# Kernel optimization log

Hardware: AMD Instinct MI355X
Metric: run time of the kernel (lower is better)

The kernel has to match this reference:

```python
import jax, jax.numpy as jnp
import numpy as np

C = 1024
FACTOR = 4
C_INT = C * FACTOR


def setup_inputs() -> dict:
    key = jax.random.key(0)
    ks = jax.random.split(key, 6)
    act = jax.random.normal(ks[0], (4, 2048, C), dtype=jnp.float32)
    mask = jnp.ones((4, 2048), dtype=jnp.float32)
    # LayerNorm params
    ln_scale = jnp.ones((C,), dtype=jnp.float32)
    ln_bias = jnp.zeros((C,), dtype=jnp.float32)
    # Linear 1 (init='linear'): lecun-normal-ish
    w1 = jax.random.normal(ks[1], (C, C_INT), dtype=jnp.float32) / np.sqrt(C)
    b1 = jnp.zeros((C_INT,), dtype=jnp.float32)
    # Linear 2 (init='final' -> zeros in AF2; use small random so grads are nontrivial)
    w2 = jax.random.normal(ks[2], (C_INT, C), dtype=jnp.float32) * 0.02
    b2 = jnp.zeros((C,), dtype=jnp.float32)
    return {"act": act, "mask": mask, "ln_scale": ln_scale, "ln_bias": ln_bias,
            "w1": w1, "b1": b1, "w2": w2, "b2": b2}


def _layernorm(x, scale, bias, eps=1e-5):
    mu = jnp.mean(x, axis=-1, keepdims=True)
    var = jnp.mean(jnp.square(x - mu), axis=-1, keepdims=True)
    return (x - mu) * jax.lax.rsqrt(var + eps) * scale + bias


def reference(act, mask, ln_scale, ln_bias, w1, b1, w2, b2):
    # mask is accepted but unused, matching the original forward.
    x = _layernorm(act, ln_scale, ln_bias)
    h = jax.nn.relu(jnp.einsum('bsc,cf->bsf', x, w1) + b1)
    return jnp.einsum('bsf,fc->bsc', h, w2) + b2
```

## Files before the change

### kernel.cpp

```cpp
#include <hip/hip_runtime.h>
#include <hip/hip_bf16.h>
#include <cstdint>

typedef unsigned short u16;
typedef __bf16 bf16x8 __attribute__((ext_vector_type(8)));
typedef float floatx4 __attribute__((ext_vector_type(4)));

#define AS1 __attribute__((address_space(1)))
#define AS3 __attribute__((address_space(3)))

static __device__ __forceinline__ u16 f2bf(float f) {
    union { float f; unsigned int u; } v; v.f = f;
    unsigned int u = v.u;
    return (u16)((u + 0x7FFFu + ((u >> 16) & 1u)) >> 16);
}

static __device__ __forceinline__ void bar() {
    __builtin_amdgcn_sched_barrier(0);
    asm volatile("" ::: "memory");
    __builtin_amdgcn_s_barrier();
    asm volatile("" ::: "memory");
    __builtin_amdgcn_sched_barrier(0);
}

__device__ __forceinline__ void transpose_body(
    const float* __restrict__ in, u16* __restrict__ out,
    int R, int Ccols, int bx, int by, int tid, float (*tile)[33])
{
    const int tx = tid & 31;
    const int ty = tid >> 5;
    const int c0 = bx * 32;
    const int r0 = by * 32;
#pragma unroll
    for (int i = 0; i < 32; i += 8)
        tile[ty + i][tx] = in[(size_t)(r0 + ty + i) * Ccols + (c0 + tx)];
    __syncthreads();
#pragma unroll
    for (int i = 0; i < 32; i += 8)
        out[(size_t)(c0 + ty + i) * R + (r0 + tx)] = f2bf(tile[tx][ty + i]);
}

__global__ __launch_bounds__(256)
void prep(const float* __restrict__ w1, const float* __restrict__ w2,
          const float* __restrict__ act, const float* __restrict__ ln_scale,
          const float* __restrict__ ln_bias,
          u16* __restrict__ W1t, u16* __restrict__ W2t, u16* __restrict__ X)
{
    __shared__ float smem[32][33];
    const int id  = blockIdx.x;
    const int tid = threadIdx.x;

    if (id < 4096) {
        transpose_body(w1, W1t, 1024, 4096, id & 127, id >> 7, tid, smem);
        return;
    }
    if (id < 8192) {
        const int t = id - 4096;
        transpose_body(w2, W2t, 4096, 1024, t & 31, t >> 5, tid, smem);
        return;
    }
    const int row = id - 8192;
    const float4 v = ((const float4*)(act + (size_t)row * 1024))[tid];
    float s  = v.x + v.y + v.z + v.w;
    float ss = v.x * v.x + v.y * v.y + v.z * v.z + v.w * v.w;
#pragma unroll
    for (int off = 32; off > 0; off >>= 1) {
        s  += __shfl_xor(s, off, 64);
        ss += __shfl_xor(ss, off, 64);
    }
    float* red = &smem[0][0];
    const int wave = tid >> 6, lane = tid & 63;
    if (lane == 0) { red[wave] = s; red[4 + wave] = ss; }
    __syncthreads();
    s  = red[0] + red[1] + red[2] + red[3];
    ss = red[4] + red[5] + red[6] + red[7];
    const float mu  = s * (1.0f / 1024.0f);
    const float var = ss * (1.0f / 1024.0f) - mu * mu;
    const float rs  = rsqrtf(var + 1e-5f);
    const float4 sc = ((const float4*)ln_scale)[tid];
    const float4 bi = ((const float4*)ln_bias)[tid];
    ushort4 o;
    o.x = f2bf((v.x - mu) * rs * sc.x + bi.x);
    o.y = f2bf((v.y - mu) * rs * sc.y + bi.y);
    o.z = f2bf((v.z - mu) * rs * sc.z + bi.z);
    o.w = f2bf((v.w - mu) * rs * sc.w + bi.w);
    ((ushort4*)(X + (size_t)row * 1024))[tid] = o;
}

template <bool BF16_OUT, bool RELU>
__global__ __launch_bounds__(512, 2)
void gemm256(const u16* __restrict__ A,
             const u16* __restrict__ Bt,
             const float* __restrict__ bias,
             void* __restrict__ Cout,
             int M, int N, int K)
{
    constexpr int BM = 256, BN = 128, BK = 64;
    constexpr int ASZ = BM * BK;
    constexpr int BSZ = BN * BK;
    __shared__ __align__(16) u16 Alds[3 * ASZ];
    __shared__ __align__(16) u16 Blds[3 * BSZ];

    const int tid  = threadIdx.x;
    const int wave = tid >> 6;
    const int lane = tid & 63;
    const int srow = lane >> 3;
    const int s_st = lane & 7;
    const int quad = lane >> 4;
    const int l16  = lane & 15;
    const int rkey = l16 & 7;
    const int wm   = wave >> 1;
    const int wn   = wave & 1;

    const int nbm = M >> 8;
    const int id  = blockIdx.x;
    const int bm  = id % nbm;
    const int bn  = id / nbm;

    const u16* Ag = A  + (size_t)bm * BM * K;
    const u16* Bg = Bt + (size_t)bn * BN * K;

    auto stageA = [&](int r, int k0, int ab) {
        const int ca  = wave * 4 + r;
        const int row = ca * 8 + srow;
        const int col = (s_st ^ (row & 7)) * 8;
        __builtin_amdgcn_global_load_lds(
            (AS1 void*)(Ag + (size_t)row * K + k0 + col),
            (AS3 void*)(&Alds[ab + ca * 512]), 16, 0, 0);
    };
    auto stageB = [&](int r, int k0, int bb) {
        const int cb  = wave * 2 + r;
        const int row = cb * 8 + srow;
        const int col = (s_st ^ (row & 7)) * 8;
        __builtin_amdgcn_global_load_lds(
            (AS1 void*)(Bg + (size_t)row * K + k0 + col),
            (AS3 void*)(&Blds[bb + cb * 512]), 16, 0, 0);
    };

    floatx4 acc[4][4];
#pragma unroll
    for (int i = 0; i < 4; ++i)
#pragma unroll
        for (int j = 0; j < 4; ++j)
            acc[i][j] = (floatx4){0.f, 0.f, 0.f, 0.f};

    const int NT = K >> 6;

#pragma unroll
    for (int r = 0; r < 4; ++r) stageA(r, 0, 0);
#pragma unroll
    for (int r = 0; r < 2; ++r) stageB(r, 0, 0);
#pragma unroll
    for (int r = 0; r < 4; ++r) stageA(r, BK, ASZ);
#pragma unroll
    for (int r = 0; r < 2; ++r) stageB(r, BK, BSZ);
    asm volatile("s_waitcnt vmcnt(6)" ::: "memory");
    bar();

    int bsel = 0;
    for (int t = 0; t < NT; ++t) {
        const int ab  = bsel * ASZ;
        const int bb  = bsel * BSZ;
        const int bs2 = (bsel >= 1) ? bsel - 1 : 2;
        const int ab2 = bs2 * ASZ;
        const int bb2 = bs2 * BSZ;
        const bool do_stage = (t + 2 < NT);
        const int  k2 = (t + 2) << 6;

#pragma unroll
        for (int kk = 0; kk < 2; ++kk) {
            const int slot = ((kk * 4 + quad) ^ rkey) * 8;
            bf16x8 afr[4], bfr[4];
#pragma unroll
            for (int i = 0; i < 4; ++i) {
                afr[i] = *(const bf16x8*)
                    &Alds[ab + (wm * 64 + i * 16 + l16) * 64 + slot];
                bfr[i] = *(const bf16x8*)
                    &Blds[bb + (wn * 64 + i * 16 + l16) * 64 + slot];
            }
            if (do_stage) {
                stageA(kk * 2 + 0, k2, ab2);
                stageA(kk * 2 + 1, k2, ab2);
                stageB(kk, k2, bb2);
            }
            bar();
            __builtin_amdgcn_s_setprio(1);
#pragma unroll
            for (int mi = 0; mi < 4; ++mi)
#pragma unroll
                for (int ni = 0; ni < 4; ++ni)
                    acc[mi][ni] = __builtin_amdgcn_mfma_f32_16x16x32_bf16(
                        bfr[ni], afr[mi], acc[mi][ni], 0, 0, 0);
            __builtin_amdgcn_s_setprio(0);
            if (kk == 1) {
                if (do_stage)
                    asm volatile("s_waitcnt vmcnt(6)" ::: "memory");
                else if (t + 1 < NT)
                    asm volatile("s_waitcnt vmcnt(0)" ::: "memory");
            }
            bar();
        }
        bsel = (bsel == 2) ? 0 : bsel + 1;
    }

    const int mbase = bm * BM + wm * 64;
    const int nbase = bn * BN + wn * 64;
#pragma unroll
    for (int mi = 0; mi < 4; ++mi) {
        const int m = mbase + mi * 16 + l16;
#pragma unroll
        for (int ni = 0; ni < 4; ++ni) {
            const int n0 = nbase + ni * 16 + quad * 4;
            const float4 bv = *(const float4*)&bias[n0];
            float v0 = acc[mi][ni][0] + bv.x;
            float v1 = acc[mi][ni][1] + bv.y;
            float v2 = acc[mi][ni][2] + bv.z;
            float v3 = acc[mi][ni][3] + bv.w;
            if (RELU) {
                v0 = fmaxf(v0, 0.f); v1 = fmaxf(v1, 0.f);
                v2 = fmaxf(v2, 0.f); v3 = fmaxf(v3, 0.f);
            }
            if (BF16_OUT) {
                ushort4 o = { f2bf(v0), f2bf(v1), f2bf(v2), f2bf(v3) };
                *(ushort4*)&((u16*)Cout)[(size_t)m * N + n0] = o;
            } else {
                float4 o = { v0, v1, v2, v3 };
                *(float4*)&((float*)Cout)[(size_t)m * N + n0] = o;
            }
        }
    }
}

extern "C" void kernel_launch(void* const* d_in, const int* in_sizes, int n_in,
                              void* d_out, int out_size, void* d_ws, size_t ws_size,
                              hipStream_t stream)
{
    const float* act      = (const float*)d_in[0];
    const float* ln_scale = (const float*)d_in[2];
    const float* ln_bias  = (const float*)d_in[3];
    const float* w1       = (const float*)d_in[4];
    const float* b1       = (const float*)d_in[5];
    const float* w2       = (const float*)d_in[6];
    const float* b2       = (const float*)d_in[7];
    float* out = (float*)d_out;

    const int M = 8192, C = 1024, CI = 4096;

    u16* X   = (u16*)d_ws;
    u16* W1t = X   + (size_t)M * C;
    u16* W2t = W1t + (size_t)CI * C;
    u16* H   = W2t + (size_t)C * CI;

    prep<<<16384, 256, 0, stream>>>(w1, w2, act, ln_scale, ln_bias, W1t, W2t, X);
    gemm256<true, true><<<(M / 256) * (CI / 128), 512, 0, stream>>>(
        X, W1t, b1, (void*)H, M, CI, C);
    gemm256<false, false><<<(M / 256) * (C / 128), 512, 0, stream>>>(
        H, W2t, b2, (void*)out, M, C, CI);
}
```

Before: 278.4 us.

## Templatize GEMM tile width, switch to double buffering with per-tile barrier

Makes the GEMM kernel's N-tile width a template parameter and uses a 256x256 tile for the first GEMM, so each wave computes an 8x4 fragment grid with more A/B reuse. The triple-buffered pipeline with two barriers per K-step and partial vmcnt waits is replaced by a double buffer: the next tile is prefetched at the start of each iteration, followed by a full vmcnt(0) wait and one barrier at the end. B fragments are held in registers across the M loop. The aim is higher arithmetic intensity and fewer barriers. The cost is more accumulator registers, less overlap of loads with compute, and fewer blocks for the first GEMM.

```diff
diff --git a/kernel.cpp b/kernel.cpp
--- a/kernel.cpp
+++ b/kernel.cpp
@@ -87,19 +87,27 @@
     ((ushort4*)(X + (size_t)row * 1024))[tid] = o;
 }
 
-template <bool BF16_OUT, bool RELU>
+template <int BN, bool BF16_OUT, bool RELU>
 __global__ __launch_bounds__(512, 2)
-void gemm256(const u16* __restrict__ A,
+void gemm_v8(const u16* __restrict__ A,
              const u16* __restrict__ Bt,
              const float* __restrict__ bias,
              void* __restrict__ Cout,
              int M, int N, int K)
 {
-    constexpr int BM = 256, BN = 128, BK = 64;
-    constexpr int ASZ = BM * BK;
-    constexpr int BSZ = BN * BK;
-    __shared__ __align__(16) u16 Alds[3 * ASZ];
-    __shared__ __align__(16) u16 Blds[3 * BSZ];
+    constexpr int BM   = 256, BK = 64;
+    constexpr int WN   = BN / 64;
+    constexpr int WM   = 8 / WN;
+    constexpr int WTM  = BM / WM;
+    constexpr int MF_M = WTM / 16;
+    constexpr int MF_N = 4;
+    constexpr int ASZ  = BM * BK;
+    constexpr int BSZ  = BN * BK;
+    constexpr int NCA  = BM / 64;
+    constexpr int NCB  = BN / 64;
+
+    __shared__ __align__(16) u16 Alds[2 * ASZ];
+    __shared__ __align__(16) u16 Blds[2 * BSZ];
 
     const int tid  = threadIdx.x;
     const int wave = tid >> 6;
@@ -109,8 +117,8 @@
     const int quad = lane >> 4;
     const int l16  = lane & 15;
     const int rkey = l16 & 7;
-    const int wm   = wave >> 1;
-    const int wn   = wave & 1;
+    const int wm   = wave / WN;
+    const int wn   = wave % WN;
 
     const int nbm = M >> 8;
     const int id  = blockIdx.x;
@@ -121,7 +129,7 @@
     const u16* Bg = Bt + (size_t)bn * BN * K;
 
     auto stageA = [&](int r, int k0, int ab) {
-        const int ca  = wave * 4 + r;
+        const int ca  = wave * NCA + r;
         const int row = ca * 8 + srow;
         const int col = (s_st ^ (row & 7)) * 8;
         __builtin_amdgcn_global_load_lds(
@@ -129,7 +137,7 @@
             (AS3 void*)(&Alds[ab + ca * 512]), 16, 0, 0);
     };
     auto stageB = [&](int r, int k0, int bb) {
-        const int cb  = wave * 2 + r;
+        const int cb  = wave * NCB + r;
         const int row = cb * 8 + srow;
         const int col = (s_st ^ (row & 7)) * 8;
         __builtin_amdgcn_global_load_lds(
@@ -137,79 +145,79 @@
             (AS3 void*)(&Blds[bb + cb * 512]), 16, 0, 0);
     };
 
-    floatx4 acc[4][4];
-#pragma unroll
-    for (int i = 0; i < 4; ++i)
-#pragma unroll
-        for (int j = 0; j < 4; ++j)
+    floatx4 acc[MF_M][MF_N];
+#pragma unroll
+    for (int i = 0; i < MF_M; ++i)
+#pragma unroll
+        for (int j = 0; j < MF_N; ++j)
             acc[i][j] = (floatx4){0.f, 0.f, 0.f, 0.f};
 
     const int NT = K >> 6;
 
 #pragma unroll
-    for (int r = 0; r < 4; ++r) stageA(r, 0, 0);
-#pragma unroll
-    for (int r = 0; r < 2; ++r) stageB(r, 0, 0);
-#pragma unroll
-    for (int r = 0; r < 4; ++r) stageA(r, BK, ASZ);
-#pragma unroll
-    for (int r = 0; r < 2; ++r) stageB(r, BK, BSZ);
-    asm volatile("s_waitcnt vmcnt(6)" ::: "memory");
+    for (int r = 0; r < NCA; ++r) stageA(r, 0, 0);
+#pragma unroll
+    for (int r = 0; r < NCB; ++r) stageB(r, 0, 0);
+    asm volatile("s_waitcnt vmcnt(0)" ::: "memory");
     bar();
 
-    int bsel = 0;
     for (int t = 0; t < NT; ++t) {
-        const int ab  = bsel * ASZ;
-        const int bb  = bsel * BSZ;
-        const int bs2 = (bsel >= 1) ? bsel - 1 : 2;
-        const int ab2 = bs2 * ASZ;
-        const int bb2 = bs2 * BSZ;
-        const bool do_stage = (t + 2 < NT);
-        const int  k2 = (t + 2) << 6;
-
-#pragma unroll
-        for (int kk = 0; kk < 2; ++kk) {
-            const int slot = ((kk * 4 + quad) ^ rkey) * 8;
-            bf16x8 afr[4], bfr[4];
-#pragma unroll
-            for (int i = 0; i < 4; ++i) {
-                afr[i] = *(const bf16x8*)
-                    &Alds[ab + (wm * 64 + i * 16 + l16) * 64 + slot];
-                bfr[i] = *(const bf16x8*)
-                    &Blds[bb + (wn * 64 + i * 16 + l16) * 64 + slot];
+        const int cur = t & 1;
+        const int ab  = cur * ASZ;
+        const int bb  = cur * BSZ;
+
+        if (t + 1 < NT) {
+            const int k1  = (t + 1) << 6;
+            const int ab2 = (cur ^ 1) * ASZ;
+            const int bb2 = (cur ^ 1) * BSZ;
+#pragma unroll
+            for (int r = 0; r < NCA; ++r) stageA(r, k1, ab2);
+#pragma unroll
+            for (int r = 0; r < NCB; ++r) stageB(r, k1, bb2);
+        }
+
+        bf16x8 bres[MF_N][2];
+#pragma unroll
+        for (int ni = 0; ni < MF_N; ++ni) {
+            const int brow = wn * 64 + ni * 16 + l16;
+#pragma unroll
+            for (int kh = 0; kh < 2; ++kh) {
+                const int slot = ((kh * 4 + quad) ^ rkey) * 8;
+                bres[ni][kh] = *(const bf16x8*)&Blds[bb + brow * BK + slot];
             }
-            if (do_stage) {
-                stageA(kk * 2 + 0, k2, ab2);
-                stageA(kk * 2 + 1, k2, ab2);
-                stageB(kk, k2, bb2);
-            }
-            bar();
+        }
+
+#pragma unroll
+        for (int mi = 0; mi < MF_M; ++mi) {
+            const int arow = wm * WTM + mi * 16 + l16;
+            const int sl0  = ((0 * 4 + quad) ^ rkey) * 8;
+            const int sl1  = ((1 * 4 + quad) ^ rkey) * 8;
+            const bf16x8 a0 = *(const bf16x8*)&Alds[ab + arow * BK + sl0];
+            const bf16x8 a1 = *(const bf16x8*)&Alds[ab + arow * BK + sl1];
             __builtin_amdgcn_s_setprio(1);
 #pragma unroll
-            for (int mi = 0; mi < 4; ++mi)
-#pragma unroll
-                for (int ni = 0; ni < 4; ++ni)
-                    acc[mi][ni] = __builtin_amdgcn_mfma_f32_16x16x32_bf16(
-                        bfr[ni], afr[mi], acc[mi][ni], 0, 0, 0);
+            for (int ni = 0; ni < MF_N; ++ni)
+                acc[mi][ni] = __builtin_amdgcn_mfma_f32_16x16x32_bf16(
+                    bres[ni][0], a0, acc[mi][ni], 0, 0, 0);
+#pragma unroll
+            for (int ni = 0; ni < MF_N; ++ni)
+                acc[mi][ni] = __builtin_amdgcn_mfma_f32_16x16x32_bf16(
+                    bres[ni][1], a1, acc[mi][ni], 0, 0, 0);
             __builtin_amdgcn_s_setprio(0);
-            if (kk == 1) {
-                if (do_stage)
-                    asm volatile("s_waitcnt vmcnt(6)" ::: "memory");
-                else if (t + 1 < NT)
-                    asm volatile("s_waitcnt vmcnt(0)" ::: "memory");
-            }
-            bar();
-        }
-        bsel = (bsel == 2) ? 0 : bsel + 1;
-    }
-
-    const int mbase = bm * BM + wm * 64;
+        }
+
+        if (t + 1 < NT)
+            asm volatile("s_waitcnt vmcnt(0)" ::: "memory");
+        bar();
+    }
+
+    const int mbase = bm * BM + wm * WTM;
     const int nbase = bn * BN + wn * 64;
 #pragma unroll
-    for (int mi = 0; mi < 4; ++mi) {
+    for (int mi = 0; mi < MF_M; ++mi) {
         const int m = mbase + mi * 16 + l16;
 #pragma unroll
-        for (int ni = 0; ni < 4; ++ni) {
+        for (int ni = 0; ni < MF_N; ++ni) {
             const int n0 = nbase + ni * 16 + quad * 4;
             const float4 bv = *(const float4*)&bias[n0];
             float v0 = acc[mi][ni][0] + bv.x;
@@ -252,8 +260,8 @@
     u16* H   = W2t + (size_t)C * CI;
 
     prep<<<16384, 256, 0, stream>>>(w1, w2, act, ln_scale, ln_bias, W1t, W2t, X);
-    gemm256<true, true><<<(M / 256) * (CI / 128), 512, 0, stream>>>(
+    gemm_v8<256, true, true><<<(M / 256) * (CI / 256), 512, 0, stream>>>(
         X, W1t, b1, (void*)H, M, CI, C);
-    gemm256<false, false><<<(M / 256) * (C / 128), 512, 0, stream>>>(
+    gemm_v8<128, false, false><<<(M / 256) * (C / 128), 512, 0, stream>>>(
         H, W2t, b2, (void*)out, M, C, CI);
 }
```

Result: slower. 286.9 us (+3.1%).
